# Optimization experiments

Hardware: AMD Instinct MI355X
Metric: run time of the kernel (lower is better)

Reference implementation:

```python
import jax, jax.numpy as jnp
import numpy as np

TEMP = 0.2
EPS = 1e-12


def _l2norm(v, axis=1):
    n = jnp.linalg.norm(v, axis=axis, keepdims=True)
    return v / jnp.maximum(n, EPS)


def setup_inputs() -> dict:
    key = jax.random.key(0)
    ks = jax.random.split(key, 7)
    B, D, P, K = 2048, 256, 100, 30
    return {
        "x": jax.random.normal(ks[0], (B, D), jnp.float32),
        "x_aug": jax.random.normal(ks[1], (B, D), jnp.float32),
        "proto_w": jax.random.normal(ks[2], (P, D), jnp.float32),
        "hard_q1": jax.random.randint(ks[3], (B,), 0, P, jnp.int32),
        "hard_q2": jax.random.randint(ks[4], (B,), 0, P, jnp.int32),
        "neg_q1": jax.random.randint(ks[5], (B, K), 0, P, jnp.int32),
        "neg_q2": jax.random.randint(ks[6], (B, K), 0, P, jnp.int32),
    }


def reference(x, x_aug, proto_w, hard_q1, hard_q2, neg_q1, neg_q2):
    B = x.shape[0]
    N = 2 * B
    P = proto_w.shape[0]

    out1 = _l2norm(x)                          # [B, D]
    out2 = _l2norm(x_aug)                      # [B, D]
    out = jnp.concatenate([out1, out2], axis=0)  # [N, D]
    hard_q = jnp.concatenate([hard_q1, hard_q2], axis=0)  # [N]
    neg_q = jnp.concatenate([neg_q1, neg_q2], axis=0)     # [N, K]

    sim = jnp.exp(jnp.matmul(out, out.T) / TEMP)  # [N, N]
    eye = jnp.eye(N, dtype=bool)

    # hard_selection: mask[i,j] = (i != j) and (hard_q[j] in neg_q[i])
    # build per-row prototype membership table [N, P] to avoid a [N, K, N] blowup
    member = jnp.zeros((N, P), dtype=bool).at[jnp.arange(N)[:, None], neg_q].set(True)
    mask = (~eye) & member[:, hard_q]  # member[i, hard_q[j]] -> [N, N]

    # sample_reweighting
    w = _l2norm(proto_w)                # normalized prototypes [P, D]
    proto_dist = jnp.matmul(w, w.T)     # cosine similarity [P, P]
    R = proto_dist[hard_q[:, None], hard_q[None, :]]  # [N, N]
    R = jnp.where(eye, 0.0, R)          # diag is 0 when the row min is taken
    rmin = jnp.min(R, axis=1, keepdims=True)
    R = jnp.where(eye, rmin, R)         # reweight[i][i] = min(reweight[i])
    rmax = jnp.max(R, axis=1, keepdims=True)
    R = (R - rmin) / (rmax - rmin)      # per-row min-max normalize
    mu = jnp.mean(R, axis=1, keepdims=True)
    std = jnp.std(R, axis=1, ddof=1, keepdims=True)  # torch.std is unbiased
    reweight = jnp.exp((R - mu) ** 2 / (2.0 * std ** 2))
    sim = sim * reweight

    # masked_select(...).sum() == global sum over masked entries (scalar)
    total = jnp.sum(jnp.where(mask, sim, 0.0))

    pos = jnp.exp(jnp.sum(out1 * out2, axis=-1) / TEMP)  # [B]
    pos = jnp.concatenate([pos, pos], axis=0)            # [N]
    loss = jnp.mean(-jnp.log(pos / total))
    return loss
```

## Files before the change

### kernel.cpp

```cpp
#include <hip/hip_runtime.h>
#include <hip/hip_bf16.h>
#include <cstdint>

#define B_ 2048
#define N_ 4096
#define D_ 256
#define P_ 100
#define K_ 30
#define INVT 5.0f

typedef __attribute__((ext_vector_type(8))) short bf16x8;
typedef __attribute__((ext_vector_type(4))) float f32x4;
typedef __attribute__((ext_vector_type(4))) unsigned short us4;

__device__ __forceinline__ float waveReduceSum(float v) {
#pragma unroll
  for (int off = 32; off > 0; off >>= 1) v += __shfl_xor(v, off, 64);
  return v;
}

__device__ __forceinline__ float blockReduceSum256(float v, float* s4) {
  int lane = threadIdx.x & 63, w = threadIdx.x >> 6;
  v = waveReduceSum(v);
  __syncthreads();
  if (lane == 0) s4[w] = v;
  __syncthreads();
  return s4[0] + s4[1] + s4[2] + s4[3];
}

__device__ __forceinline__ unsigned short f2bf(float f) {
  __hip_bfloat16 h = __float2bfloat16(f);
  return *reinterpret_cast<unsigned short*>(&h);
}
__device__ __forceinline__ float bf2f(unsigned short u) {
  return __uint_as_float(((unsigned int)u) << 16);
}

__global__ void prep_kernel(const float* __restrict__ pw, const int* __restrict__ hq1,
                            const int* __restrict__ hq2, int* __restrict__ hq,
                            int* __restrict__ cnt, float* __restrict__ pninv,
                            float* __restrict__ sums) {
  __shared__ int c[P_];
  __shared__ float s4[4];
  int t = threadIdx.x;
  if (blockIdx.x == 0) {
    if (t < 2) sums[t] = 0.f;
    if (t < P_) c[t] = 0;
    __syncthreads();
    for (int i = t; i < N_; i += 256) {
      int q = (i < B_) ? hq1[i] : hq2[i - B_];
      hq[i] = q;
      atomicAdd(&c[q], 1);
    }
    __syncthreads();
    if (t < P_) cnt[t] = c[t];
  } else {
    int r = blockIdx.x - 1;
    float a = pw[r * D_ + t];
    float ss = blockReduceSum256(a * a, s4);
    if (t == 0) pninv[r] = 1.f / fmaxf(sqrtf(ss), 1e-12f);
  }
}

__global__ void normpd_kernel(const float* __restrict__ x, const float* __restrict__ xa,
                              const float* __restrict__ pw, const float* __restrict__ pninv,
                              __hip_bfloat16* __restrict__ outb, float* __restrict__ pd,
                              float* __restrict__ sums) {
  __shared__ float s4[4];
  __shared__ float wq[D_];
  int t = threadIdx.x, lane = t & 63, wv = t >> 6;
  if (blockIdx.x < 512) {
    int i = blockIdx.x * 4 + wv;
    float4 a = ((const float4*)(x + i * D_))[lane];
    float ss = waveReduceSum(a.x * a.x + a.y * a.y + a.z * a.z + a.w * a.w);
    float inv1 = 1.f / fmaxf(sqrtf(ss), 1e-12f);
    float o1x = a.x * inv1, o1y = a.y * inv1, o1z = a.z * inv1, o1w = a.w * inv1;
    us4 p1; p1[0] = f2bf(o1x); p1[1] = f2bf(o1y); p1[2] = f2bf(o1z); p1[3] = f2bf(o1w);
    ((us4*)(outb + i * D_))[lane] = p1;
    float4 b = ((const float4*)(xa + i * D_))[lane];
    float ss2 = waveReduceSum(b.x * b.x + b.y * b.y + b.z * b.z + b.w * b.w);
    float inv2 = 1.f / fmaxf(sqrtf(ss2), 1e-12f);
    float o2x = b.x * inv2, o2y = b.y * inv2, o2z = b.z * inv2, o2w = b.w * inv2;
    us4 p2; p2[0] = f2bf(o2x); p2[1] = f2bf(o2y); p2[2] = f2bf(o2z); p2[3] = f2bf(o2w);
    ((us4*)(outb + (B_ + i) * D_))[lane] = p2;
    float d = waveReduceSum(o1x * o2x + o1y * o2y + o1z * o2z + o1w * o2w);
    if (lane == 0) s4[wv] = d;
    __syncthreads();
    if (t == 0) atomicAdd(&sums[1], s4[0] + s4[1] + s4[2] + s4[3]);
  } else {
    int q = blockIdx.x - 512;
    wq[t] = pw[q * D_ + t];
    __syncthreads();
    float nq = pninv[q];
    for (int r = wv; r < P_; r += 4) {
      float4 b = ((const float4*)(pw + r * D_))[lane];
      float s = wq[lane * 4] * b.x + wq[lane * 4 + 1] * b.y +
                wq[lane * 4 + 2] * b.z + wq[lane * 4 + 3] * b.w;
      s = waveReduceSum(s);
      if (lane == 0) pd[q * P_ + r] = s * nq * pninv[r];
    }
  }
}

__global__ void gtab_kernel(const int* __restrict__ hq, const int* __restrict__ cnt,
                            const float* __restrict__ pd, const int* __restrict__ nq1,
                            const int* __restrict__ nq2, unsigned short* __restrict__ gtabh) {
  __shared__ unsigned char memb[4][104];
  int wv = threadIdx.x >> 6, lane = threadIdx.x & 63;
  int i = blockIdx.x * 4 + wv;
  int q = hq[i];
  if (lane < 52) { memb[wv][lane * 2] = 0; memb[wv][lane * 2 + 1] = 0; }
  __syncthreads();
  const int* nrow = (i < B_) ? (nq1 + i * K_) : (nq2 + (i - B_) * K_);
  if (lane < K_) memb[wv][nrow[lane]] = 1;
  __syncthreads();

  int p0 = lane, p1 = lane + 64;
  bool has1 = (p1 < P_);
  float v0 = pd[q * P_ + p0];
  int m0 = cnt[p0] - (p0 == q ? 1 : 0);
  float v1 = 0.f; int m1 = 0;
  if (has1) { v1 = pd[q * P_ + p1]; m1 = cnt[p1] - (p1 == q ? 1 : 0); }

  float mn = 1e30f, mx = -1e30f;
  if (m0 > 0) { mn = fminf(mn, v0); mx = fmaxf(mx, v0); }
  if (has1 && m1 > 0) { mn = fminf(mn, v1); mx = fmaxf(mx, v1); }
#pragma unroll
  for (int off = 32; off > 0; off >>= 1) {
    mn = fminf(mn, __shfl_xor(mn, off, 64));
    mx = fmaxf(mx, __shfl_xor(mx, off, 64));
  }
  float rmin = fminf(0.f, mn);
  float rmax = fmaxf(rmin, mx);
  float inv = 1.f / (rmax - rmin);
  float r0 = (v0 - rmin) * inv, r1 = (v1 - rmin) * inv;
  float s1 = (m0 > 0 ? (float)m0 * r0 : 0.f) + ((has1 && m1 > 0) ? (float)m1 * r1 : 0.f);
  s1 = waveReduceSum(s1);
  float mu = s1 / (float)N_;
  float ss = (m0 > 0 ? (float)m0 * (r0 - mu) * (r0 - mu) : 0.f) +
             ((has1 && m1 > 0) ? (float)m1 * (r1 - mu) * (r1 - mu) : 0.f);
  ss = waveReduceSum(ss);
  ss += mu * mu;
  float var = ss / (float)(N_ - 1);
  float i2v = 1.f / (2.f * var);
  float g0 = memb[wv][p0] ? __expf((r0 - mu) * (r0 - mu) * i2v) : 0.f;
  gtabh[i * P_ + p0] = f2bf(g0);
  if (has1) {
    float g1 = memb[wv][p1] ? __expf((r1 - mu) * (r1 - mu) * i2v) : 0.f;
    gtabh[i * P_ + p1] = f2bf(g1);
  }
}

__device__ __forceinline__ void gload16(void* ldsdst, const void* gsrc) {
  __builtin_amdgcn_global_load_lds(
      (const __attribute__((address_space(1))) unsigned int*)gsrc,
      (__attribute__((address_space(3))) unsigned int*)ldsdst, 16, 0, 0);
}

__global__ __launch_bounds__(512, 2) void tot_kernel(
    const __hip_bfloat16* __restrict__ outb, const unsigned short* __restrict__ gtabh,
    const int* __restrict__ hq, float* __restrict__ sums) {
  __shared__ __align__(16) char lds[65536];
  __shared__ float s8[8];
  const int tid = threadIdx.x, lane = tid & 63, wid = tid >> 6;

  int rem = blockIdx.x, bi = 0;
  while (rem >= 32 - bi) { rem -= 32 - bi; ++bi; }
  const int bj = bi + rem;
  const bool offdiag = (bi != bj);
  const int i0 = bi * 128, j0 = bj * 128;
  const int wr = wid >> 2, wc = wid & 3;

  f32x4 acc[4][2] = {};

  const int wseg = wid & 3;
  const bool isB = (wid >= 4);
  const int growbase = isB ? j0 : i0;
  char* panel = lds + (isB ? 32768 : 0);

  for (int kk = 0; kk < 2; ++kk) {
#pragma unroll
    for (int it = 0; it < 8; ++it) {
      int rbase = wseg * 32 + it * 4;
      int row = rbase + (lane >> 4);
      int c = lane & 15;
      int src = (growbase + row) * D_ + kk * 128 + ((c ^ (row & 7)) * 8);
      gload16(panel + rbase * 256, outb + src);
    }
    __syncthreads();
#pragma unroll
    for (int ks = 0; ks < 4; ++ks) {
      bf16x8 af[4], bfr[2];
#pragma unroll
      for (int m = 0; m < 4; ++m) {
        int row = wr * 64 + m * 16 + (lane & 15);
        int off = row * 256 + ((((ks << 2) + (lane >> 4)) ^ (row & 7)) << 4);
        af[m] = *(const bf16x8*)(lds + off);
      }
#pragma unroll
      for (int n = 0; n < 2; ++n) {
        int row = wc * 32 + n * 16 + (lane & 15);
        int off = 32768 + row * 256 + ((((ks << 2) + (lane >> 4)) ^ (row & 7)) << 4);
        bfr[n] = *(const bf16x8*)(lds + off);
      }
#pragma unroll
      for (int m = 0; m < 4; ++m)
#pragma unroll
        for (int n = 0; n < 2; ++n)
          acc[m][n] = __builtin_amdgcn_mfma_f32_16x16x32_bf16(af[m], bfr[n], acc[m][n], 0, 0, 0);
    }
    __syncthreads();
  }

  unsigned short* ga = (unsigned short*)lds;
  unsigned short* gb = (unsigned short*)(lds + 26624);
  int* hqA = (int*)(lds + 53248);
  int* hqB = (int*)(lds + 53760);
  for (int idx = tid; idx < 128 * P_; idx += 512) {
    int r = idx / P_, c = idx - r * P_;
    ga[r * 104 + c] = gtabh[(i0 + r) * P_ + c];
    gb[r * 104 + c] = gtabh[(j0 + r) * P_ + c];
  }
  if (tid < 128) hqA[tid] = hq[i0 + tid];
  else if (tid < 256) hqB[tid - 128] = hq[j0 + tid - 128];
  __syncthreads();

  const int jl0 = wc * 32 + (lane & 15);
  const int jl1 = jl0 + 16;
  const int hj0 = hqB[jl0], hj1 = hqB[jl1];
  float local = 0.f;
#pragma unroll
  for (int m = 0; m < 4; ++m) {
    int ilb = wr * 64 + m * 16 + ((lane >> 4) << 2);
#pragma unroll
    for (int r = 0; r < 4; ++r) {
      int il = ilb + r;
      float e0 = __expf(acc[m][0][r] * INVT);
      float e1 = __expf(acc[m][1][r] * INVT);
      float wa0 = bf2f(ga[il * 104 + hj0]);
      float wa1 = bf2f(ga[il * 104 + hj1]);
      if (offdiag) {
        int hi = hqA[il];
        float wb0 = bf2f(gb[jl0 * 104 + hi]);
        float wb1 = bf2f(gb[jl1 * 104 + hi]);
        local += (wa0 + wb0) * e0 + (wa1 + wb1) * e1;
      } else {
        if (il != jl0) local += wa0 * e0;
        if (il != jl1) local += wa1 * e1;
      }
    }
  }
  local = waveReduceSum(local);
  if (lane == 0) s8[wid] = local;
  __syncthreads();
  if (tid == 0) {
    float t = 0.f;
#pragma unroll
    for (int w = 0; w < 8; ++w) t += s8[w];
    atomicAdd(&sums[0], t);
  }
}

__global__ void finish_kernel(const float* __restrict__ sums, float* __restrict__ out) {
  out[0] = logf(sums[0]) - sums[1] * (INVT / (float)B_);
}

extern "C" void kernel_launch(void* const* d_in, const int* in_sizes, int n_in,
                              void* d_out, int out_size, void* d_ws, size_t ws_size,
                              hipStream_t stream) {
  const float* x   = (const float*)d_in[0];
  const float* xa  = (const float*)d_in[1];
  const float* pw  = (const float*)d_in[2];
  const int* hq1   = (const int*)d_in[3];
  const int* hq2   = (const int*)d_in[4];
  const int* nq1   = (const int*)d_in[5];
  const int* nq2   = (const int*)d_in[6];
  float* out = (float*)d_out;

  char* ws = (char*)d_ws;
  __hip_bfloat16* outb  = (__hip_bfloat16*)(ws);
  unsigned short* gtabh = (unsigned short*)(ws + 2097152);
  float* pd    = (float*)(ws + 2916352);
  float* pninv = (float*)(ws + 2956352);
  int*   hq    = (int*)  (ws + 2956800);
  int*   cnt   = (int*)  (ws + 2973184);
  float* sums  = (float*)(ws + 2973696);

  prep_kernel<<<101, 256, 0, stream>>>(pw, hq1, hq2, hq, cnt, pninv, sums);
  normpd_kernel<<<612, 256, 0, stream>>>(x, xa, pw, pninv, outb, pd, sums);
  gtab_kernel<<<N_ / 4, 256, 0, stream>>>(hq, cnt, pd, nq1, nq2, gtabh);
  tot_kernel<<<528, 512, 0, stream>>>(outb, gtabh, hq, sums);
  finish_kernel<<<1, 1, 0, stream>>>(sums, out);
}
```

Baseline: 126.1 us.

## Merge prep kernels, use full tile grid, fuse finish via last-block ticket

Merges the prototype-norm and normalization/prototype-distance kernels into one launch that computes norms inline. The tot kernel now runs over the full 32x32 tile grid instead of the upper triangle, so each tile reads only a transposed gtab slice for row weights and does vectorized lookups. The finish kernel becomes a last-block ticket inside tot_kernel. Together these cut launch overhead and per-element LDS work, but double the MFMA work, and the occupancy hint is raised to 4 blocks per SM even though the 64KB LDS use likely limits that.

```diff
diff --git a/kernel.cpp b/kernel.cpp
--- a/kernel.cpp
+++ b/kernel.cpp
@@ -19,15 +19,6 @@
   return v;
 }
 
-__device__ __forceinline__ float blockReduceSum256(float v, float* s4) {
-  int lane = threadIdx.x & 63, w = threadIdx.x >> 6;
-  v = waveReduceSum(v);
-  __syncthreads();
-  if (lane == 0) s4[w] = v;
-  __syncthreads();
-  return s4[0] + s4[1] + s4[2] + s4[3];
-}
-
 __device__ __forceinline__ unsigned short f2bf(float f) {
   __hip_bfloat16 h = __float2bfloat16(f);
   return *reinterpret_cast<unsigned short*>(&h);
@@ -36,15 +27,18 @@
   return __uint_as_float(((unsigned int)u) << 16);
 }
 
-__global__ void prep_kernel(const float* __restrict__ pw, const int* __restrict__ hq1,
-                            const int* __restrict__ hq2, int* __restrict__ hq,
-                            int* __restrict__ cnt, float* __restrict__ pninv,
-                            float* __restrict__ sums) {
+__global__ __launch_bounds__(256) void prep_kernel(
+    const float* __restrict__ x, const float* __restrict__ xa, const float* __restrict__ pw,
+    const int* __restrict__ hq1, const int* __restrict__ hq2, int* __restrict__ hq,
+    int* __restrict__ cnt, float* __restrict__ pd, __hip_bfloat16* __restrict__ outb,
+    float* __restrict__ sums) {
   __shared__ int c[P_];
   __shared__ float s4[4];
-  int t = threadIdx.x;
-  if (blockIdx.x == 0) {
+  int t = threadIdx.x, lane = t & 63, wv = t >> 6;
+  int bx = blockIdx.x;
+  if (bx == 0) {
     if (t < 2) sums[t] = 0.f;
+    if (t == 2) ((int*)sums)[2] = 0;
     if (t < P_) c[t] = 0;
     __syncthreads();
     for (int i = t; i < N_; i += 256) {
@@ -54,23 +48,21 @@
     }
     __syncthreads();
     if (t < P_) cnt[t] = c[t];
+  } else if (bx <= P_) {
+    int q = bx - 1;
+    float4 aq = ((const float4*)(pw + q * D_))[lane];
+    float ssq = waveReduceSum(aq.x * aq.x + aq.y * aq.y + aq.z * aq.z + aq.w * aq.w);
+    float qinv = 1.f / fmaxf(sqrtf(ssq), 1e-12f);
+    for (int r = wv; r < P_; r += 4) {
+      float4 b = ((const float4*)(pw + r * D_))[lane];
+      float s = aq.x * b.x + aq.y * b.y + aq.z * b.z + aq.w * b.w;
+      float n = b.x * b.x + b.y * b.y + b.z * b.z + b.w * b.w;
+      s = waveReduceSum(s);
+      n = waveReduceSum(n);
+      if (lane == 0) pd[q * P_ + r] = s * qinv / fmaxf(sqrtf(n), 1e-12f);
+    }
   } else {
-    int r = blockIdx.x - 1;
-    float a = pw[r * D_ + t];
-    float ss = blockReduceSum256(a * a, s4);
-    if (t == 0) pninv[r] = 1.f / fmaxf(sqrtf(ss), 1e-12f);
-  }
-}
-
-__global__ void normpd_kernel(const float* __restrict__ x, const float* __restrict__ xa,
-                              const float* __restrict__ pw, const float* __restrict__ pninv,
-                              __hip_bfloat16* __restrict__ outb, float* __restrict__ pd,
-                              float* __restrict__ sums) {
-  __shared__ float s4[4];
-  __shared__ float wq[D_];
-  int t = threadIdx.x, lane = t & 63, wv = t >> 6;
-  if (blockIdx.x < 512) {
-    int i = blockIdx.x * 4 + wv;
+    int i = (bx - 101) * 4 + wv;
     float4 a = ((const float4*)(x + i * D_))[lane];
     float ss = waveReduceSum(a.x * a.x + a.y * a.y + a.z * a.z + a.w * a.w);
     float inv1 = 1.f / fmaxf(sqrtf(ss), 1e-12f);
@@ -87,18 +79,6 @@
     if (lane == 0) s4[wv] = d;
     __syncthreads();
     if (t == 0) atomicAdd(&sums[1], s4[0] + s4[1] + s4[2] + s4[3]);
-  } else {
-    int q = blockIdx.x - 512;
-    wq[t] = pw[q * D_ + t];
-    __syncthreads();
-    float nq = pninv[q];
-    for (int r = wv; r < P_; r += 4) {
-      float4 b = ((const float4*)(pw + r * D_))[lane];
-      float s = wq[lane * 4] * b.x + wq[lane * 4 + 1] * b.y +
-                wq[lane * 4 + 2] * b.z + wq[lane * 4 + 3] * b.w;
-      s = waveReduceSum(s);
-      if (lane == 0) pd[q * P_ + r] = s * nq * pninv[r];
-    }
   }
 }
 
@@ -157,18 +137,13 @@
       (__attribute__((address_space(3))) unsigned int*)ldsdst, 16, 0, 0);
 }
 
-__global__ __launch_bounds__(512, 2) void tot_kernel(
+__global__ __launch_bounds__(512, 4) void tot_kernel(
     const __hip_bfloat16* __restrict__ outb, const unsigned short* __restrict__ gtabh,
-    const int* __restrict__ hq, float* __restrict__ sums) {
+    const int* __restrict__ hq, float* __restrict__ sums, float* __restrict__ out) {
   __shared__ __align__(16) char lds[65536];
   __shared__ float s8[8];
   const int tid = threadIdx.x, lane = tid & 63, wid = tid >> 6;
-
-  int rem = blockIdx.x, bi = 0;
-  while (rem >= 32 - bi) { rem -= 32 - bi; ++bi; }
-  const int bj = bi + rem;
-  const bool offdiag = (bi != bj);
-  const int i0 = bi * 128, j0 = bj * 128;
+  const int i0 = blockIdx.y * 128, j0 = blockIdx.x * 128;
   const int wr = wid >> 2, wc = wid & 3;
 
   f32x4 acc[4][2] = {};
@@ -212,42 +187,32 @@
     __syncthreads();
   }
 
-  unsigned short* ga = (unsigned short*)lds;
-  unsigned short* gb = (unsigned short*)(lds + 26624);
-  int* hqA = (int*)(lds + 53248);
-  int* hqB = (int*)(lds + 53760);
+  unsigned short* gaT = (unsigned short*)lds;
+  int* hqj = (int*)(lds + 26624);
   for (int idx = tid; idx < 128 * P_; idx += 512) {
     int r = idx / P_, c = idx - r * P_;
-    ga[r * 104 + c] = gtabh[(i0 + r) * P_ + c];
-    gb[r * 104 + c] = gtabh[(j0 + r) * P_ + c];
-  }
-  if (tid < 128) hqA[tid] = hq[i0 + tid];
-  else if (tid < 256) hqB[tid - 128] = hq[j0 + tid - 128];
+    gaT[c * 132 + r] = gtabh[(i0 + r) * P_ + c];
+  }
+  if (tid < 128) hqj[tid] = hq[j0 + tid];
   __syncthreads();
 
   const int jl0 = wc * 32 + (lane & 15);
   const int jl1 = jl0 + 16;
-  const int hj0 = hqB[jl0], hj1 = hqB[jl1];
+  const int hj0 = hqj[jl0], hj1 = hqj[jl1];
+  const int jg0 = j0 + jl0, jg1 = j0 + jl1;
   float local = 0.f;
 #pragma unroll
   for (int m = 0; m < 4; ++m) {
     int ilb = wr * 64 + m * 16 + ((lane >> 4) << 2);
+    us4 w0 = *(const us4*)(gaT + hj0 * 132 + ilb);
+    us4 w1 = *(const us4*)(gaT + hj1 * 132 + ilb);
 #pragma unroll
     for (int r = 0; r < 4; ++r) {
-      int il = ilb + r;
+      int ig = i0 + ilb + r;
       float e0 = __expf(acc[m][0][r] * INVT);
       float e1 = __expf(acc[m][1][r] * INVT);
-      float wa0 = bf2f(ga[il * 104 + hj0]);
-      float wa1 = bf2f(ga[il * 104 + hj1]);
-      if (offdiag) {
-        int hi = hqA[il];
-        float wb0 = bf2f(gb[jl0 * 104 + hi]);
-        float wb1 = bf2f(gb[jl1 * 104 + hi]);
-        local += (wa0 + wb0) * e0 + (wa1 + wb1) * e1;
-      } else {
-        if (il != jl0) local += wa0 * e0;
-        if (il != jl1) local += wa1 * e1;
-      }
+      local += (ig != jg0) ? bf2f(w0[r]) * e0 : 0.f;
+      local += (ig != jg1) ? bf2f(w1[r]) * e1 : 0.f;
     }
   }
   local = waveReduceSum(local);
@@ -258,11 +223,15 @@
 #pragma unroll
     for (int w = 0; w < 8; ++w) t += s8[w];
     atomicAdd(&sums[0], t);
-  }
-}
-
-__global__ void finish_kernel(const float* __restrict__ sums, float* __restrict__ out) {
-  out[0] = logf(sums[0]) - sums[1] * (INVT / (float)B_);
+    __threadfence();
+    int* ticket = (int*)sums + 2;
+    int done = atomicAdd(ticket, 1);
+    if (done == 1023) {
+      float tot = atomicAdd(&sums[0], 0.f);
+      float pos = atomicAdd(&sums[1], 0.f);
+      out[0] = logf(tot) - pos * (INVT / (float)B_);
+    }
+  }
 }
 
 extern "C" void kernel_launch(void* const* d_in, const int* in_sizes, int n_in,
@@ -281,14 +250,11 @@
   __hip_bfloat16* outb  = (__hip_bfloat16*)(ws);
   unsigned short* gtabh = (unsigned short*)(ws + 2097152);
   float* pd    = (float*)(ws + 2916352);
-  float* pninv = (float*)(ws + 2956352);
   int*   hq    = (int*)  (ws + 2956800);
   int*   cnt   = (int*)  (ws + 2973184);
   float* sums  = (float*)(ws + 2973696);
 
-  prep_kernel<<<101, 256, 0, stream>>>(pw, hq1, hq2, hq, cnt, pninv, sums);
-  normpd_kernel<<<612, 256, 0, stream>>>(x, xa, pw, pninv, outb, pd, sums);
+  prep_kernel<<<613, 256, 0, stream>>>(x, xa, pw, hq1, hq2, hq, cnt, pd, outb, sums);
   gtab_kernel<<<N_ / 4, 256, 0, stream>>>(hq, cnt, pd, nq1, nq2, gtabh);
-  tot_kernel<<<528, 512, 0, stream>>>(outb, gtabh, hq, sums);
-  finish_kernel<<<1, 1, 0, stream>>>(sums, out);
-}
+  tot_kernel<<<dim3(32, 32), 512, 0, stream>>>(outb, gtabh, hq, sums, out);
+}
```

Result: slower. 132.7 us (+5.2%).
